# Optimization experiments

Measured on AMD Instinct MI355X. Metric: run time of the kernel, lower is better.

The kernel has to match this reference:

```python
import jax, jax.numpy as jnp
import numpy as np

C = 512
B, H, W = 4, 64, 64
GROUPS = 32
EPS = 1e-6
SCALE = 1.0 / np.sqrt(C)


def setup_inputs() -> dict:
    key = jax.random.key(0)
    ks = jax.random.split(key, 3)
    x = jax.random.normal(ks[0], (B, C, H, W), dtype=jnp.float32)
    # conv weights: kaiming-ish small init for numerical sanity
    qkv_w = jax.random.normal(ks[1], (3 * C, C), dtype=jnp.float32) * (1.0 / np.sqrt(C))
    proj_w = jax.random.normal(ks[2], (C, C), dtype=jnp.float32) * (1.0 / np.sqrt(C))
    return {
        "x": x,
        "norm_w": jnp.ones((C,), jnp.float32),
        "norm_b": jnp.zeros((C,), jnp.float32),
        "qkv_w": qkv_w,
        "qkv_b": jnp.zeros((3 * C,), jnp.float32),
        "proj_w": proj_w,
        "proj_b": jnp.zeros((C,), jnp.float32),
    }


def reference(x, norm_w, norm_b, qkv_w, qkv_b, proj_w, proj_b):
    b, c, h, w = x.shape
    hw = h * w
    # GroupNorm(32, eps=1e-6, affine)
    xg = x.reshape(b, GROUPS, -1)                       # [B, G, (C/G)*H*W]
    mean = jnp.mean(xg, axis=-1, keepdims=True)
    var = jnp.var(xg, axis=-1, keepdims=True)
    xn = ((xg - mean) * jax.lax.rsqrt(var + EPS)).reshape(b, c, h, w)
    xn = xn * norm_w[:, None, None] + norm_b[:, None, None]
    # 1x1 conv qkv == channel matmul
    qkv = jnp.einsum('oc,bchw->bohw', qkv_w, xn) + qkv_b[:, None, None]
    q, k, v = jnp.split(qkv, 3, axis=1)                 # each [B, C, H, W]
    q = q.reshape(b, c, hw)                              # [B, C, HW]
    k = k.reshape(b, c, hw)
    v = v.reshape(b, c, hw)
    # attn[b, i, j] = softmax_j( q_i . k_j * scale )
    scores = jnp.einsum('bci,bcj->bij', q, k) * SCALE    # [B, HW, HW]
    attn = jax.nn.softmax(scores, axis=-1)
    # h[b, c, i] = sum_j v[b, c, j] * attn[b, i, j]
    hmap = jnp.einsum('bcj,bij->bci', v, attn).reshape(b, c, h, w)
    out = x + jnp.einsum('oc,bchw->bohw', proj_w, hmap) + proj_b[:, None, None]
    return out
```

## Files before the change

kernel.cpp:

```cpp
#include <hip/hip_runtime.h>
#include <hip/hip_fp8.h>
#include <cstdint>
#include <cmath>

#define B_   4
#define C_   512
#define HW_  4096
#define G_   32
#define CPG_ 16
#define EPS_ 1e-6f
#define SCALE_ 0.04419417382415922f
#define PSCALE_ 0.0625f


typedef __bf16 bf16_t;
typedef __bf16 bf16x8 __attribute__((ext_vector_type(8)));
typedef __bf16 bf16x4 __attribute__((ext_vector_type(4)));
typedef float  f32x4  __attribute__((ext_vector_type(4)));
typedef int    i32x4  __attribute__((ext_vector_type(4)));
typedef int    i32x8  __attribute__((ext_vector_type(8)));
typedef unsigned int u32;
typedef __hip_fp8_e4m3 fp8_t;

__device__ __forceinline__ void cp16(const void* g, void* l) {
  __builtin_amdgcn_global_load_lds((__attribute__((address_space(1))) u32*)(g),
                                   (__attribute__((address_space(3))) u32*)(l),
                                   16, 0, 0);
}

__device__ __forceinline__ void zero_acc(f32x4 acc[4][4]) {
  f32x4 z = {0.f, 0.f, 0.f, 0.f};
#pragma unroll
  for (int i = 0; i < 4; ++i)
#pragma unroll
    for (int j = 0; j < 4; ++j) acc[i][j] = z;
}

__device__ __forceinline__ void gemm_bt64(const bf16_t* __restrict__ A,
                                          const bf16_t* __restrict__ B,
                                          int K, int lda, int ldb,
                                          f32x4 acc[4][4]) {
  __shared__ __align__(16) bf16_t As[128 * 64];
  __shared__ __align__(16) bf16_t Bs[128 * 64];
  const int tid  = threadIdx.x;
  const int wave = tid >> 6;
  const int lane = tid & 63;
  const int wm = (wave >> 1) * 64;
  const int wn = (wave & 1) * 64;
  const int srow = lane >> 3;
  const int gch  = ((lane & 7) - srow) & 7;
  const bf16_t* gA = A + (size_t)(wave * 32 + srow) * lda + gch * 8;
  const bf16_t* gB = B + (size_t)(wave * 32 + srow) * ldb + gch * 8;
  bf16_t* lA = As + wave * 32 * 64;
  bf16_t* lB = Bs + wave * 32 * 64;
  const int fr = lane & 15;
  const int q  = lane >> 4;
  const int eo0 = ((q + fr) & 7) * 8;
  const int eo1 = ((q + 4 + fr) & 7) * 8;

  for (int k0 = 0; k0 < K; k0 += 64) {
#pragma unroll
    for (int cc = 0; cc < 4; ++cc) {
      cp16(gA + (size_t)(cc * 8) * lda, lA + cc * 512);
      cp16(gB + (size_t)(cc * 8) * ldb, lB + cc * 512);
    }
    gA += 64; gB += 64;
    __syncthreads();
#pragma unroll
    for (int h = 0; h < 2; ++h) {
      const int eo = h ? eo1 : eo0;
      bf16x8 a[4], b[4];
#pragma unroll
      for (int i = 0; i < 4; ++i)
        a[i] = *(const bf16x8*)(As + (wm + i * 16 + fr) * 64 + eo);
#pragma unroll
      for (int j = 0; j < 4; ++j)
        b[j] = *(const bf16x8*)(Bs + (wn + j * 16 + fr) * 64 + eo);
#pragma unroll
      for (int i = 0; i < 4; ++i)
#pragma unroll
        for (int j = 0; j < 4; ++j)
          acc[i][j] = __builtin_amdgcn_mfma_f32_16x16x32_bf16(a[i], b[j], acc[i][j], 0, 0, 0);
    }
    __syncthreads();
  }
}

template <bool ROWSUM>
__device__ __forceinline__ void gemm_bt_mx(const unsigned char* __restrict__ A,
                                           const unsigned char* __restrict__ B,
                                           int K, int lda, int ldb,
                                           f32x4 acc[4][4], f32x4 accl[4]) {
  __shared__ __align__(16) unsigned char As[128 * 128];
  __shared__ __align__(16) unsigned char Bs[128 * 128];
  const int tid  = threadIdx.x;
  const int wave = tid >> 6;
  const int lane = tid & 63;
  const int wm = (wave >> 1) * 64;
  const int wn = (wave & 1) * 64;
  const int srow = lane >> 3;
  const int gch  = ((lane & 7) - srow) & 7;
  const unsigned char* gA = A + (size_t)(wave * 32 + srow) * lda + gch * 16;
  const unsigned char* gB = B + (size_t)(wave * 32 + srow) * ldb + gch * 16;
  unsigned char* lA = As + wave * 32 * 128;
  unsigned char* lB = Bs + wave * 32 * 128;
  const int fr = lane & 15;
  const int q  = lane >> 4;
  const int co0 = ((2 * q     + fr) & 7) * 16;
  const int co1 = ((2 * q + 1 + fr) & 7) * 16;
  const i32x8 vones = {0x38383838, 0x38383838, 0x38383838, 0x38383838,
                       0x38383838, 0x38383838, 0x38383838, 0x38383838};

  for (int k0 = 0; k0 < K; k0 += 128) {
#pragma unroll
    for (int cc = 0; cc < 4; ++cc) {
      cp16(gA + (size_t)(cc * 8) * lda, lA + cc * 1024);
      cp16(gB + (size_t)(cc * 8) * ldb, lB + cc * 1024);
    }
    gA += 128; gB += 128;
    __syncthreads();
    i32x8 a[4], b[4];
#pragma unroll
    for (int i = 0; i < 4; ++i) {
      const int ro = (wm + i * 16 + fr) * 128;
      i32x4 lo = *(const i32x4*)(As + ro + co0);
      i32x4 hi = *(const i32x4*)(As + ro + co1);
      a[i] = __builtin_shufflevector(lo, hi, 0, 1, 2, 3, 4, 5, 6, 7);
    }
#pragma unroll
    for (int j = 0; j < 4; ++j) {
      const int ro = (wn + j * 16 + fr) * 128;
      i32x4 lo = *(const i32x4*)(Bs + ro + co0);
      i32x4 hi = *(const i32x4*)(Bs + ro + co1);
      b[j] = __builtin_shufflevector(lo, hi, 0, 1, 2, 3, 4, 5, 6, 7);
    }
#pragma unroll
    for (int i = 0; i < 4; ++i) {
#pragma unroll
      for (int j = 0; j < 4; ++j)
        acc[i][j] = __builtin_amdgcn_mfma_scale_f32_16x16x128_f8f6f4(
            a[i], b[j], acc[i][j], 0, 0, 0, 0x7F, 0, 0x7F);
      if (ROWSUM)
        accl[i] = __builtin_amdgcn_mfma_scale_f32_16x16x128_f8f6f4(
            a[i], vones, accl[i], 0, 0, 0, 0x7F, 0, 0x7F);
    }
    __syncthreads();
  }
}


__global__ void __launch_bounds__(256) cast_w_kernel(const float* __restrict__ qkv_w,
                                                     const float* __restrict__ proj_w,
                                                     bf16_t* __restrict__ wqkv,
                                                     bf16_t* __restrict__ wproj) {
  int idx = blockIdx.x * 256 + threadIdx.x;
  const int nq = 1536 * 512;
  if (idx < nq) {
    wqkv[idx] = (bf16_t)qkv_w[idx];
  } else {
    int t = idx - nq;
    int p = t & 511;
    int off = p & 63;
    int c = (p & ~63) + ((off & 3) << 4) + (off >> 2);
    wproj[t] = (bf16_t)proj_w[(t & ~511) + c];
  }
}

__global__ void __launch_bounds__(256) gn_partial_kernel(const float* __restrict__ x,
                                                         float* __restrict__ stats) {
  __shared__ float rs[256], rss[256];
  const int bg = blockIdx.x >> 3;
  const int ch = blockIdx.x & 7;
  const float4* base = (const float4*)(x + (size_t)bg * (CPG_ * HW_)) +
                       (size_t)ch * (CPG_ * HW_ / 4 / 8);
  float s = 0.f, ss = 0.f;
  for (int i = threadIdx.x; i < CPG_ * HW_ / 4 / 8; i += 256) {
    float4 v = base[i];
    s  += v.x + v.y + v.z + v.w;
    ss += v.x * v.x + v.y * v.y + v.z * v.z + v.w * v.w;
  }
  rs[threadIdx.x] = s; rss[threadIdx.x] = ss;
  __syncthreads();
  for (int st = 128; st > 0; st >>= 1) {
    if ((int)threadIdx.x < st) {
      rs[threadIdx.x]  += rs[threadIdx.x + st];
      rss[threadIdx.x] += rss[threadIdx.x + st];
    }
    __syncthreads();
  }
  if (threadIdx.x == 0) {
    atomicAdd(&stats[bg * 2 + 0], rs[0]);
    atomicAdd(&stats[bg * 2 + 1], rss[0]);
  }
}

__global__ void __launch_bounds__(128) gn_final_kernel(float* __restrict__ stats) {
  const int bg = threadIdx.x;
  const float inv = 1.f / (float)(CPG_ * HW_);
  float mean = stats[bg * 2 + 0] * inv;
  float var  = stats[bg * 2 + 1] * inv - mean * mean;
  stats[bg * 2 + 0] = mean;
  stats[bg * 2 + 1] = rsqrtf(var + EPS_);
}

__global__ void __launch_bounds__(256) norm_tr_kernel(const float* __restrict__ x,
                                                      const float* __restrict__ stats,
                                                      const float* __restrict__ nw,
                                                      const float* __restrict__ nb,
                                                      bf16_t* __restrict__ xnT) {
  __shared__ float tile[64][65];
  const int b  = blockIdx.z;
  const int i0 = blockIdx.x * 64;
  const int c0 = blockIdx.y * 64;
  const int tx = threadIdx.x & 63;
  const int ty = threadIdx.x >> 6;
  const int cbase = c0 + ty * 16;
  const int g = cbase >> 4;
  const float mean = stats[(b * G_ + g) * 2 + 0];
  const float rstd = stats[(b * G_ + g) * 2 + 1];
#pragma unroll
  for (int r = 0; r < 16; ++r) {
    const int c = cbase + r;
    float v = x[((size_t)b * C_ + c) * HW_ + i0 + tx];
    tile[ty * 16 + r][tx] = (v - mean) * rstd * nw[c] + nb[c];
  }
  __syncthreads();
#pragma unroll
  for (int r = 0; r < 16; ++r) {
    const int il = ty * 16 + r;
    xnT[((size_t)b * HW_ + i0 + il) * C_ + c0 + tx] = (bf16_t)tile[tx][il];
  }
}


__global__ void __launch_bounds__(256) qk_gemm_kernel(const bf16_t* __restrict__ xnT,
                                                      const bf16_t* __restrict__ wqkv,
                                                      const float* __restrict__ qkv_b,
                                                      fp8_t* __restrict__ QKt8) {
  const int b = blockIdx.z;
  f32x4 acc[4][4]; zero_acc(acc);
  const bf16_t* A  = xnT + ((size_t)b * HW_ + blockIdx.y * 128) * C_;
  const bf16_t* Bp = wqkv + (size_t)blockIdx.x * 128 * C_;
  gemm_bt64(A, Bp, C_, C_, C_, acc);
  const int lane = threadIdx.x & 63, wave = threadIdx.x >> 6;
  const int wm = (wave >> 1) * 64, wn = (wave & 1) * 64;
  const int fr = lane & 15, q = lane >> 4;
  const int r0 = blockIdx.y * 128 + wm + (q << 2);
  const int cb = blockIdx.x * 128 + wn;
  float bias[4];
#pragma unroll
  for (int j = 0; j < 4; ++j) bias[j] = qkv_b[cb + fr + j * 16];
#pragma unroll
  for (int i = 0; i < 4; ++i)
#pragma unroll
    for (int r = 0; r < 4; ++r) {
      const int row = r0 + i * 16 + r;
      u32 dw = 0;
      dw = (u32)__builtin_amdgcn_cvt_pk_fp8_f32(acc[i][0][r] + bias[0],
                                                acc[i][1][r] + bias[1], (int)dw, false);
      dw = (u32)__builtin_amdgcn_cvt_pk_fp8_f32(acc[i][2][r] + bias[2],
                                                acc[i][3][r] + bias[3], (int)dw, true);
      *(u32*)((unsigned char*)QKt8 + ((size_t)b * HW_ + row) * 1024 + cb + fr * 4) = dw;
    }
}

__global__ void __launch_bounds__(256) v_gemm_kernel(const bf16_t* __restrict__ wqkv,
                                                     const bf16_t* __restrict__ xnT,
                                                     const float* __restrict__ qkv_b,
                                                     fp8_t* __restrict__ V8) {
  const int b = blockIdx.z;
  f32x4 acc[4][4]; zero_acc(acc);
  const bf16_t* A  = wqkv + (size_t)(1024 + blockIdx.y * 128) * C_;
  const bf16_t* Bp = xnT + ((size_t)b * HW_ + blockIdx.x * 128) * C_;
  gemm_bt64(A, Bp, C_, C_, C_, acc);
  const int lane = threadIdx.x & 63, wave = threadIdx.x >> 6;
  const int wm = (wave >> 1) * 64, wn = (wave & 1) * 64;
  const int fr = lane & 15, q = lane >> 4;
  const int r0 = blockIdx.y * 128 + wm + (q << 2);
  const int cb = blockIdx.x * 128 + wn;
#pragma unroll
  for (int i = 0; i < 4; ++i)
#pragma unroll
    for (int r = 0; r < 4; ++r) {
      const int row = r0 + i * 16 + r;
      const float bias = qkv_b[1024 + row];
      u32 dw = 0;
      dw = (u32)__builtin_amdgcn_cvt_pk_fp8_f32(acc[i][0][r] + bias,
                                                acc[i][1][r] + bias, (int)dw, false);
      dw = (u32)__builtin_amdgcn_cvt_pk_fp8_f32(acc[i][2][r] + bias,
                                                acc[i][3][r] + bias, (int)dw, true);
      *(u32*)((unsigned char*)V8 + ((size_t)b * C_ + row) * HW_ + cb + fr * 4) = dw;
    }
}

__global__ void __launch_bounds__(256) sexp_gemm_kernel(const fp8_t* __restrict__ QKt8,
                                                        fp8_t* __restrict__ P8) {
  const int b = blockIdx.z;
  const unsigned char* QKtb = (const unsigned char*)QKt8 + (size_t)b * HW_ * 1024;
  fp8_t* Pb = P8 + (size_t)b * HW_ * HW_;
  f32x4 acc[4][4]; zero_acc(acc);
  const unsigned char* A  = QKtb + (size_t)blockIdx.y * 128 * 1024;
  const unsigned char* Bp = QKtb + 512 + (size_t)blockIdx.x * 128 * 1024;
  gemm_bt_mx<false>(A, Bp, 512, 1024, 1024, acc, nullptr);
  const int lane = threadIdx.x & 63, wave = threadIdx.x >> 6;
  const int wm = (wave >> 1) * 64, wn = (wave & 1) * 64;
  const int fr = lane & 15, q = lane >> 4;
  const int r0 = blockIdx.y * 128 + wm + (q << 2);
  const int cb = blockIdx.x * 128 + wn;
#pragma unroll
  for (int i = 0; i < 4; ++i)
#pragma unroll
    for (int r = 0; r < 4; ++r) {
      const int row = r0 + i * 16 + r;
      float e0 = __expf(acc[i][0][r] * SCALE_) * PSCALE_;
      float e1 = __expf(acc[i][1][r] * SCALE_) * PSCALE_;
      float e2 = __expf(acc[i][2][r] * SCALE_) * PSCALE_;
      float e3 = __expf(acc[i][3][r] * SCALE_) * PSCALE_;
      u32 dw = 0;
      dw = (u32)__builtin_amdgcn_cvt_pk_fp8_f32(e0, e1, (int)dw, false);
      dw = (u32)__builtin_amdgcn_cvt_pk_fp8_f32(e2, e3, (int)dw, true);
      *(u32*)((unsigned char*)Pb + (size_t)row * HW_ + cb + fr * 4) = dw;
    }
}

__global__ void __launch_bounds__(256) pv_gemm_kernel(const fp8_t* __restrict__ P8,
                                                      const fp8_t* __restrict__ V8,
                                                      bf16_t* __restrict__ hmT) {
  const int n   = blockIdx.x;
  const int xcd = n & 7;
  const int p   = n >> 3;
  const int xb  = p & 3;
  const int grp = xcd * 16 + (p >> 2);
  const int yb  = grp & 31;
  const int b   = grp >> 5;

  const unsigned char* A  = (const unsigned char*)P8 + (size_t)b * HW_ * HW_ +
                            (size_t)yb * 128 * HW_;
  const unsigned char* Bp = (const unsigned char*)V8 + (size_t)b * C_ * HW_ +
                            (size_t)xb * 128 * HW_;
  bf16_t* hmTb = hmT + (size_t)b * HW_ * C_;

  f32x4 acc[4][4]; zero_acc(acc);
  f32x4 accl[4];
  {
    f32x4 z = {0.f, 0.f, 0.f, 0.f};
#pragma unroll
    for (int i = 0; i < 4; ++i) accl[i] = z;
  }
  gemm_bt_mx<true>(A, Bp, HW_, HW_, HW_, acc, accl);

  const int lane = threadIdx.x & 63, wave = threadIdx.x >> 6;
  const int wm = (wave >> 1) * 64, wn = (wave & 1) * 64;
  const int fr = lane & 15, q = lane >> 4;
  const int r0 = yb * 128 + wm + (q << 2);
  const int cb = xb * 128 + wn;
#pragma unroll
  for (int i = 0; i < 4; ++i)
#pragma unroll
    for (int r = 0; r < 4; ++r) {
      const int row = r0 + i * 16 + r;
      const float rl = 1.f / accl[i][r];
      bf16x4 o;
#pragma unroll
      for (int j = 0; j < 4; ++j) o[j] = (bf16_t)(acc[i][j][r] * rl);
      *(bf16x4*)(hmTb + (size_t)row * C_ + cb + fr * 4) = o;
    }
}

__global__ void __launch_bounds__(256) proj_gemm_kernel(const bf16_t* __restrict__ wproj,
                                                        const bf16_t* __restrict__ hmT,
                                                        const float* __restrict__ proj_b,
                                                        const float* __restrict__ x,
                                                        float* __restrict__ out) {
  const int b = blockIdx.z;
  f32x4 acc[4][4]; zero_acc(acc);
  const bf16_t* A  = wproj + (size_t)blockIdx.y * 128 * C_;
  const bf16_t* Bp = hmT + ((size_t)b * HW_ + blockIdx.x * 128) * C_;
  gemm_bt64(A, Bp, C_, C_, C_, acc);
  const int lane = threadIdx.x & 63, wave = threadIdx.x >> 6;
  const int wm = (wave >> 1) * 64, wn = (wave & 1) * 64;
  const int r0 = blockIdx.y * 128 + wm + ((lane >> 4) << 2);
  const int c0 = blockIdx.x * 128 + wn + (lane & 15);
#pragma unroll
  for (int i = 0; i < 4; ++i)
#pragma unroll
    for (int r = 0; r < 4; ++r) {
      const int row = r0 + i * 16 + r;
      const float bias = proj_b[row];
#pragma unroll
      for (int j = 0; j < 4; ++j) {
        const int col = c0 + j * 16;
        const size_t idx = ((size_t)b * C_ + row) * HW_ + col;
        out[idx] = x[idx] + bias + acc[i][j][r];
      }
    }
}

extern "C" void kernel_launch(void* const* d_in, const int* in_sizes, int n_in,
                              void* d_out, int out_size, void* d_ws, size_t ws_size,
                              hipStream_t stream) {
  const float* x      = (const float*)d_in[0];
  const float* norm_w = (const float*)d_in[1];
  const float* norm_b = (const float*)d_in[2];
  const float* qkv_w  = (const float*)d_in[3];
  const float* qkv_b  = (const float*)d_in[4];
  const float* proj_w = (const float*)d_in[5];
  const float* proj_b = (const float*)d_in[6];
  float* out = (float*)d_out;

  char* ws = (char*)d_ws;
  size_t o = 0;
  bf16_t* wqkv  = (bf16_t*)(ws + o); o += (size_t)1536 * 512 * 2;
  bf16_t* wproj = (bf16_t*)(ws + o); o += (size_t)512 * 512 * 2;
  float*  stats = (float*)(ws + o);  o += 128 * 2 * 4;
  bf16_t* xnT   = (bf16_t*)(ws + o); o += (size_t)B_ * HW_ * C_ * 2;
  fp8_t*  QKt8  = (fp8_t*)(ws + o);  o += (size_t)B_ * HW_ * 1024;
  fp8_t*  V8    = (fp8_t*)(ws + o);  o += (size_t)B_ * C_ * HW_;
  bf16_t* hmT   = (bf16_t*)(ws + o); o += (size_t)B_ * HW_ * C_ * 2;
  fp8_t*  P8    = (fp8_t*)(ws + o);  o += (size_t)B_ * HW_ * HW_;

  cast_w_kernel<<<4096, 256, 0, stream>>>(qkv_w, proj_w, wqkv, wproj);
  hipMemsetAsync(stats, 0, 128 * 2 * sizeof(float), stream);
  gn_partial_kernel<<<1024, 256, 0, stream>>>(x, stats);
  gn_final_kernel<<<1, 128, 0, stream>>>(stats);
  norm_tr_kernel<<<dim3(HW_ / 64, C_ / 64, B_), 256, 0, stream>>>(x, stats, norm_w, norm_b, xnT);
  qk_gemm_kernel<<<dim3(1024 / 128, HW_ / 128, B_), 256, 0, stream>>>(xnT, wqkv, qkv_b, QKt8);
  v_gemm_kernel<<<dim3(HW_ / 128, C_ / 128, B_), 256, 0, stream>>>(wqkv, xnT, qkv_b, V8);
  sexp_gemm_kernel<<<dim3(HW_ / 128, HW_ / 128, B_), 256, 0, stream>>>(QKt8, P8);
  pv_gemm_kernel<<<512, 256, 0, stream>>>(P8, V8, hmT);
  proj_gemm_kernel<<<dim3(HW_ / 128, C_ / 128, B_), 256, 0, stream>>>(
      wproj, hmT, proj_b, x, out);
}
```

Before: 251.3 us.

## Load fp8 GEMM operands directly from global memory and fold GN finalize into norm

Removes the shared-memory staged fp8 GEMM helper. The score-exp and PV GEMMs now have each wave read its MFMA operand fragments straight from global memory into registers, with no LDS and no barriers. This drops the LDS round trip and synchronisation but loses cross-wave data sharing, so every wave fetches its own A/B rows from L2, which raises cache traffic for the large PV GEMM. It also folds the group-norm mean/rstd computation into the normalize kernel, removing one tiny kernel launch.

```diff
diff --git a/kernel.cpp b/kernel.cpp
--- a/kernel.cpp
+++ b/kernel.cpp
@@ -86,68 +86,6 @@
   }
 }
 
-template <bool ROWSUM>
-__device__ __forceinline__ void gemm_bt_mx(const unsigned char* __restrict__ A,
-                                           const unsigned char* __restrict__ B,
-                                           int K, int lda, int ldb,
-                                           f32x4 acc[4][4], f32x4 accl[4]) {
-  __shared__ __align__(16) unsigned char As[128 * 128];
-  __shared__ __align__(16) unsigned char Bs[128 * 128];
-  const int tid  = threadIdx.x;
-  const int wave = tid >> 6;
-  const int lane = tid & 63;
-  const int wm = (wave >> 1) * 64;
-  const int wn = (wave & 1) * 64;
-  const int srow = lane >> 3;
-  const int gch  = ((lane & 7) - srow) & 7;
-  const unsigned char* gA = A + (size_t)(wave * 32 + srow) * lda + gch * 16;
-  const unsigned char* gB = B + (size_t)(wave * 32 + srow) * ldb + gch * 16;
-  unsigned char* lA = As + wave * 32 * 128;
-  unsigned char* lB = Bs + wave * 32 * 128;
-  const int fr = lane & 15;
-  const int q  = lane >> 4;
-  const int co0 = ((2 * q     + fr) & 7) * 16;
-  const int co1 = ((2 * q + 1 + fr) & 7) * 16;
-  const i32x8 vones = {0x38383838, 0x38383838, 0x38383838, 0x38383838,
-                       0x38383838, 0x38383838, 0x38383838, 0x38383838};
-
-  for (int k0 = 0; k0 < K; k0 += 128) {
-#pragma unroll
-    for (int cc = 0; cc < 4; ++cc) {
-      cp16(gA + (size_t)(cc * 8) * lda, lA + cc * 1024);
-      cp16(gB + (size_t)(cc * 8) * ldb, lB + cc * 1024);
-    }
-    gA += 128; gB += 128;
-    __syncthreads();
-    i32x8 a[4], b[4];
-#pragma unroll
-    for (int i = 0; i < 4; ++i) {
-      const int ro = (wm + i * 16 + fr) * 128;
-      i32x4 lo = *(const i32x4*)(As + ro + co0);
-      i32x4 hi = *(const i32x4*)(As + ro + co1);
-      a[i] = __builtin_shufflevector(lo, hi, 0, 1, 2, 3, 4, 5, 6, 7);
-    }
-#pragma unroll
-    for (int j = 0; j < 4; ++j) {
-      const int ro = (wn + j * 16 + fr) * 128;
-      i32x4 lo = *(const i32x4*)(Bs + ro + co0);
-      i32x4 hi = *(const i32x4*)(Bs + ro + co1);
-      b[j] = __builtin_shufflevector(lo, hi, 0, 1, 2, 3, 4, 5, 6, 7);
-    }
-#pragma unroll
-    for (int i = 0; i < 4; ++i) {
-#pragma unroll
-      for (int j = 0; j < 4; ++j)
-        acc[i][j] = __builtin_amdgcn_mfma_scale_f32_16x16x128_f8f6f4(
-            a[i], b[j], acc[i][j], 0, 0, 0, 0x7F, 0, 0x7F);
-      if (ROWSUM)
-        accl[i] = __builtin_amdgcn_mfma_scale_f32_16x16x128_f8f6f4(
-            a[i], vones, accl[i], 0, 0, 0, 0x7F, 0, 0x7F);
-    }
-    __syncthreads();
-  }
-}
-
 
 __global__ void __launch_bounds__(256) cast_w_kernel(const float* __restrict__ qkv_w,
                                                      const float* __restrict__ proj_w,
@@ -194,15 +132,6 @@
   }
 }
 
-__global__ void __launch_bounds__(128) gn_final_kernel(float* __restrict__ stats) {
-  const int bg = threadIdx.x;
-  const float inv = 1.f / (float)(CPG_ * HW_);
-  float mean = stats[bg * 2 + 0] * inv;
-  float var  = stats[bg * 2 + 1] * inv - mean * mean;
-  stats[bg * 2 + 0] = mean;
-  stats[bg * 2 + 1] = rsqrtf(var + EPS_);
-}
-
 __global__ void __launch_bounds__(256) norm_tr_kernel(const float* __restrict__ x,
                                                       const float* __restrict__ stats,
                                                       const float* __restrict__ nw,
@@ -216,8 +145,11 @@
   const int ty = threadIdx.x >> 6;
   const int cbase = c0 + ty * 16;
   const int g = cbase >> 4;
-  const float mean = stats[(b * G_ + g) * 2 + 0];
-  const float rstd = stats[(b * G_ + g) * 2 + 1];
+  const float inv = 1.f / (float)(CPG_ * HW_);
+  const float sum  = stats[(b * G_ + g) * 2 + 0];
+  const float ssum = stats[(b * G_ + g) * 2 + 1];
+  const float mean = sum * inv;
+  const float rstd = rsqrtf(ssum * inv - mean * mean + EPS_);
 #pragma unroll
   for (int r = 0; r < 16; ++r) {
     const int c = cbase + r;
@@ -298,13 +230,34 @@
   const int b = blockIdx.z;
   const unsigned char* QKtb = (const unsigned char*)QKt8 + (size_t)b * HW_ * 1024;
   fp8_t* Pb = P8 + (size_t)b * HW_ * HW_;
+  const unsigned char* A  = QKtb + (size_t)blockIdx.y * 128 * 1024;
+  const unsigned char* Bg = QKtb + 512 + (size_t)blockIdx.x * 128 * 1024;
   f32x4 acc[4][4]; zero_acc(acc);
-  const unsigned char* A  = QKtb + (size_t)blockIdx.y * 128 * 1024;
-  const unsigned char* Bp = QKtb + 512 + (size_t)blockIdx.x * 128 * 1024;
-  gemm_bt_mx<false>(A, Bp, 512, 1024, 1024, acc, nullptr);
   const int lane = threadIdx.x & 63, wave = threadIdx.x >> 6;
   const int wm = (wave >> 1) * 64, wn = (wave & 1) * 64;
   const int fr = lane & 15, q = lane >> 4;
+  const unsigned char* pa[4];
+  const unsigned char* pb[4];
+#pragma unroll
+  for (int i = 0; i < 4; ++i) pa[i] = A  + (size_t)(wm + i * 16 + fr) * 1024 + q * 32;
+#pragma unroll
+  for (int j = 0; j < 4; ++j) pb[j] = Bg + (size_t)(wn + j * 16 + fr) * 1024 + q * 32;
+
+#pragma unroll
+  for (int kk = 0; kk < 4; ++kk) {
+    i32x8 a[4], bv[4];
+#pragma unroll
+    for (int i = 0; i < 4; ++i) a[i]  = *(const i32x8*)(pa[i] + kk * 128);
+#pragma unroll
+    for (int j = 0; j < 4; ++j) bv[j] = *(const i32x8*)(pb[j] + kk * 128);
+#pragma unroll
+    for (int i = 0; i < 4; ++i)
+#pragma unroll
+      for (int j = 0; j < 4; ++j)
+        acc[i][j] = __builtin_amdgcn_mfma_scale_f32_16x16x128_f8f6f4(
+            a[i], bv[j], acc[i][j], 0, 0, 0, 0x7F, 0, 0x7F);
+  }
+
   const int r0 = blockIdx.y * 128 + wm + (q << 2);
   const int cb = blockIdx.x * 128 + wn;
 #pragma unroll
@@ -336,7 +289,7 @@
 
   const unsigned char* A  = (const unsigned char*)P8 + (size_t)b * HW_ * HW_ +
                             (size_t)yb * 128 * HW_;
-  const unsigned char* Bp = (const unsigned char*)V8 + (size_t)b * C_ * HW_ +
+  const unsigned char* Bg = (const unsigned char*)V8 + (size_t)b * C_ * HW_ +
                             (size_t)xb * 128 * HW_;
   bf16_t* hmTb = hmT + (size_t)b * HW_ * C_;
 
@@ -347,11 +300,36 @@
 #pragma unroll
     for (int i = 0; i < 4; ++i) accl[i] = z;
   }
-  gemm_bt_mx<true>(A, Bp, HW_, HW_, HW_, acc, accl);
-
   const int lane = threadIdx.x & 63, wave = threadIdx.x >> 6;
   const int wm = (wave >> 1) * 64, wn = (wave & 1) * 64;
   const int fr = lane & 15, q = lane >> 4;
+  const unsigned char* pa[4];
+  const unsigned char* pb[4];
+#pragma unroll
+  for (int i = 0; i < 4; ++i) pa[i] = A  + (size_t)(wm + i * 16 + fr) * HW_ + q * 32;
+#pragma unroll
+  for (int j = 0; j < 4; ++j) pb[j] = Bg + (size_t)(wn + j * 16 + fr) * HW_ + q * 32;
+  const i32x8 vones = {0x38383838, 0x38383838, 0x38383838, 0x38383838,
+                       0x38383838, 0x38383838, 0x38383838, 0x38383838};
+
+#pragma unroll 4
+  for (int kk = 0; kk < 32; ++kk) {
+    i32x8 a[4], bv[4];
+#pragma unroll
+    for (int i = 0; i < 4; ++i) a[i]  = *(const i32x8*)(pa[i] + kk * 128);
+#pragma unroll
+    for (int j = 0; j < 4; ++j) bv[j] = *(const i32x8*)(pb[j] + kk * 128);
+#pragma unroll
+    for (int i = 0; i < 4; ++i) {
+#pragma unroll
+      for (int j = 0; j < 4; ++j)
+        acc[i][j] = __builtin_amdgcn_mfma_scale_f32_16x16x128_f8f6f4(
+            a[i], bv[j], acc[i][j], 0, 0, 0, 0x7F, 0, 0x7F);
+      accl[i] = __builtin_amdgcn_mfma_scale_f32_16x16x128_f8f6f4(
+          a[i], vones, accl[i], 0, 0, 0, 0x7F, 0, 0x7F);
+    }
+  }
+
   const int r0 = yb * 128 + wm + (q << 2);
   const int cb = xb * 128 + wn;
 #pragma unroll
@@ -422,7 +400,6 @@
   cast_w_kernel<<<4096, 256, 0, stream>>>(qkv_w, proj_w, wqkv, wproj);
   hipMemsetAsync(stats, 0, 128 * 2 * sizeof(float), stream);
   gn_partial_kernel<<<1024, 256, 0, stream>>>(x, stats);
-  gn_final_kernel<<<1, 128, 0, stream>>>(stats);
   norm_tr_kernel<<<dim3(HW_ / 64, C_ / 64, B_), 256, 0, stream>>>(x, stats, norm_w, norm_b, xnT);
   qk_gemm_kernel<<<dim3(1024 / 128, HW_ / 128, B_), 256, 0, stream>>>(xnT, wqkv, qkv_b, QKt8);
   v_gemm_kernel<<<dim3(HW_ / 128, C_ / 128, B_), 256, 0, stream>>>(wqkv, xnT, qkv_b, V8);
```

Result: slower. 394.6 us (+57.0%).
